# Optimization experiments

Hardware: AMD Instinct MI355X
Metric: run time of the kernel (lower is better)

Reference implementation:

```python
import jax, jax.numpy as jnp
import numpy as np
from jax import lax

IOU_THRESHOLD = 0.1
B, N = 4, 8192


def setup_inputs() -> dict:
    key = jax.random.key(0)
    # [B, 5, N]: rows 0..3 = cx, cy, w, h; row 4 = confidence score in (0, 1)
    outputs = jax.random.uniform(key, (B, 5, N), dtype=jnp.float32)
    return {"outputs": outputs}


def _nms_single(p):
    """Greedy NMS on one image. p: [5, N] -> [5, N] with kept boxes
    compacted to the front (original column order preserved) and the rest
    zero-padded. Matches the torch loop: repeatedly take the highest-scoring
    surviving box, drop all boxes with IoU >= threshold (box keeps itself),
    and drop boxes with score <= 0."""
    boxes, scores = p[:4], p[4]
    n = scores.shape[0]
    order = jnp.argsort(-scores)            # descending score order
    b = boxes[:, order]

    x1 = b[0] - b[2] * 0.5
    y1 = b[1] - b[3] * 0.5
    x2 = b[0] + b[2] * 0.5
    y2 = b[1] + b[3] * 0.5
    area = (x2 - x1) * (y2 - y1)

    iw = jnp.clip(jnp.minimum(x2[:, None], x2[None, :]) - jnp.maximum(x1[:, None], x1[None, :]), 0.0)
    ih = jnp.clip(jnp.minimum(y2[:, None], y2[None, :]) - jnp.maximum(y1[:, None], y1[None, :]), 0.0)
    inter = iw * ih
    union = area[:, None] + area[None, :] - inter
    iou = inter / (union + 1e-8)            # [N, N] in sorted order

    idx_range = jnp.arange(n)
    keep_init = scores[order] > 0           # non_zero_scores filter

    def body(i, keep):
        # if box i (in score order) survives, suppress j with IoU >= thr, j != i
        row_keep = (iou[i] < IOU_THRESHOLD) | (idx_range == i)
        return jnp.where(keep[i], keep & row_keep, keep)

    keep_sorted = lax.fori_loop(0, n, body, keep_init)

    # map keep mask back to original column order
    keep_orig = jnp.zeros((n,), bool).at[order].set(keep_sorted)
    # stable compaction: kept columns first, original relative order preserved
    perm = jnp.argsort(jnp.where(keep_orig, 0, 1), stable=True)
    gathered = p[:, perm]                    # [5, N]
    valid = idx_range < jnp.sum(keep_orig)
    return jnp.where(valid[None, :], gathered, 0.0)


def reference(outputs):
    # torch version pads to the max detections across the batch; here we keep
    # the fixed width N (extra columns are zero), same kept values/order.
    return jax.vmap(_nms_single)(outputs)


if __name__ == "__main__":
    inp = setup_inputs()
    out = jax.jit(reference)(**inp)
    print(out.shape, out.dtype)
```

## Files before the change

### kernel.cpp

```cpp
#include <hip/hip_runtime.h>

#pragma clang fp contract(off)

#define NBOX 8192
#define BLK  1024
#define EPT  8
#define NBUCK 2048
#define NB 256
#define IOU_THR 0.1f

typedef unsigned short u16;
typedef unsigned int u32;
typedef unsigned long long u64;

#define SMEM_TOT 160896

__global__ __launch_bounds__(BLK, 4) void nms_kernel(const float* __restrict__ in,
                                                     float* __restrict__ out) {
    __shared__ __align__(16) char smem[SMEM_TOT];
    const int img = blockIdx.x;
    const float* __restrict__ p = in + (size_t)img * 5 * NBOX;
    float* __restrict__ o = out + (size_t)img * 5 * NBOX;
    const int t = threadIdx.x;
    const int lane = t & 63;
    const int wid = t >> 6;

    float4* box   = (float4*)smem;
    u16* A        = (u16*)(smem + 131072);
    float4* bx    = (float4*)(smem + 147456);
    u64 (*mat)[4] = (u64(*)[4])(smem + 151552);
    float4* kx    = (float4*)(smem + 151552);
    u32* pfxA     = (u32*)(smem + 155648);
    u32* kom      = (u32*)(smem + 159744);
    int* wcnt     = (int*)(smem + 160768);
    u64* keptQ    = (u64*)(smem + 160832);
    int* S0sh     = (int*)(smem + 160864);
    u64* skey  = (u64*)smem;
    u32* hist  = (u32*)(smem + 65536);
    u32* bbase = (u32*)(smem + 73728);

    for (int i = t; i < NBUCK; i += BLK) hist[i] = 0;
    if (t < 256) kom[t] = 0;
    if (t == 0) *S0sh = 0;
    __syncthreads();

    u32 mybkt[EPT], myarr[EPT], mykeyhi[EPT];
#pragma unroll
    for (int e = 0; e < EPT; e++) {
        int j = t + e * BLK;
        float s = p[4 * NBOX + j];
        u32 u = __float_as_uint(s);
        u32 ordb = u ^ (u32)(((int)u >> 31) | (int)0x80000000);
        mykeyhi[e] = ~ordb;
        int vb = (int)(s * (float)NBUCK);
        vb = vb < 0 ? 0 : (vb > NBUCK - 1 ? NBUCK - 1 : vb);
        mybkt[e] = (u32)(NBUCK - 1 - vb);
        myarr[e] = atomicAdd(&hist[mybkt[e]], 1u);
        u64 bal = __ballot(s > 0.0f);
        if (lane == 0) atomicAdd(S0sh, (int)__popcll(bal));
    }
    __syncthreads();

    {
        u32 h0 = hist[2 * t], h1 = hist[2 * t + 1];
        int v = (int)(h0 + h1);
        int x = v;
        for (int d = 1; d < 64; d <<= 1) {
            int y = __shfl_up(x, d, 64);
            if (lane >= d) x += y;
        }
        if (lane == 63) wcnt[wid] = x;
        __syncthreads();
        int wb = 0;
        for (int i = 0; i < wid; i++) wb += wcnt[i];
        int excl = wb + x - v;
        bbase[2 * t] = (u32)excl;
        bbase[2 * t + 1] = (u32)excl + h0;
    }
    __syncthreads();

#pragma unroll
    for (int e = 0; e < EPT; e++) {
        u32 pos = bbase[mybkt[e]] + myarr[e];
        skey[pos] = ((u64)mykeyhi[e] << 32) | (u32)(t + e * BLK);
    }
    __syncthreads();

#pragma unroll
    for (int e = 0; e < EPT; e++) {
        u32 b = mybkt[e];
        u32 lo = bbase[b], hi2 = lo + hist[b];
        u64 me = ((u64)mykeyhi[e] << 32) | (u32)(t + e * BLK);
        u32 r = lo;
        for (u32 q = lo; q < hi2; q++) r += (skey[q] < me) ? 1u : 0u;
        A[r] = (u16)(t + e * BLK);
    }
    __syncthreads();
    int S = *S0sh;

#pragma unroll
    for (int e = 0; e < EPT; e++) {
        int j = t + e * BLK;
        float cx = p[j], cy = p[NBOX + j];
        float w_ = p[2 * NBOX + j], h_ = p[3 * NBOX + j];
        box[j] = make_float4(cx - w_ * 0.5f, cy - h_ * 0.5f,
                             cx + w_ * 0.5f, cy + h_ * 0.5f);
    }
    __syncthreads();

    if (t < NB) bx[t] = box[A[t]];
    __syncthreads();

    while (S > 0) {
        int nb = S < NB ? S : NB;

        {
            int i = t >> 2, ws = t & 3;
            if (i < nb) {
                float4 bi = bx[i];
                float ari = (bi.z - bi.x) * (bi.w - bi.y);
                u64 bits = 0;
                int c0 = ws * 64;
                int cmax = nb - c0; if (cmax > 64) cmax = 64;
                for (int cc = 0; cc < cmax; cc++) {
                    int c = c0 + cc;
                    float4 bc = bx[c];
                    float arc = (bc.z - bc.x) * (bc.w - bc.y);
                    float iw = fminf(bi.z, bc.z) - fmaxf(bi.x, bc.x);
                    float ih = fminf(bi.w, bc.w) - fmaxf(bi.y, bc.y);
                    if (c != i && iw > 0.0f && ih > 0.0f) {
                        float inter = iw * ih;
                        float uni = ari + arc - inter;
                        if (inter / (uni + 1e-8f) >= IOU_THR) bits |= (1ull << cc);
                    }
                }
                mat[i][ws] = bits;
            }
        }
        __syncthreads();

        if (wid == 0) {
            u64 r0[4], r1[4], r2[4], r3[4];
#pragma unroll
            for (int wq = 0; wq < 4; wq++) {
                r0[wq] = mat[lane][wq];
                r1[wq] = mat[64 + lane][wq];
                r2[wq] = mat[128 + lane][wq];
                r3[wq] = mat[192 + lane][wq];
            }
            u64 A0, A1, A2, A3;
            {
                int n0 = nb;       A0 = n0 <= 0 ? 0ull : (n0 >= 64 ? ~0ull : ((1ull << n0) - 1ull));
                int n1 = nb - 64;  A1 = n1 <= 0 ? 0ull : (n1 >= 64 ? ~0ull : ((1ull << n1) - 1ull));
                int n2 = nb - 128; A2 = n2 <= 0 ? 0ull : (n2 >= 64 ? ~0ull : ((1ull << n2) - 1ull));
                int n3 = nb - 192; A3 = n3 <= 0 ? 0ull : (n3 >= 64 ? ~0ull : ((1ull << n3) - 1ull));
            }
            u64 K0 = 0, K1 = 0, K2 = 0, K3 = 0;
            u64 lm = (1ull << lane) - 1ull;
            while (A0 | A1 | A2 | A3) {
                bool c0b = ((A0 >> lane) & 1) && !(r0[0] & A0 & lm);
                bool c1b = ((A1 >> lane) & 1) && !((r1[0] & A0) | (r1[1] & A1 & lm));
                bool c2b = ((A2 >> lane) & 1) && !((r2[0] & A0) | (r2[1] & A1) | (r2[2] & A2 & lm));
                bool c3b = ((A3 >> lane) & 1) && !((r3[0] & A0) | (r3[1] & A1) | (r3[2] & A2) | (r3[3] & A3 & lm));
                u64 C0 = __ballot(c0b), C1 = __ballot(c1b), C2 = __ballot(c2b), C3 = __ballot(c3b);
                K0 |= C0; K1 |= C1; K2 |= C2; K3 |= C3;
                A0 &= ~C0; A1 &= ~C1; A2 &= ~C2; A3 &= ~C3;
                bool s0b = ((A0 >> lane) & 1) && ((r0[0] & C0) | (r0[1] & C1) | (r0[2] & C2) | (r0[3] & C3));
                bool s1b = ((A1 >> lane) & 1) && ((r1[0] & C0) | (r1[1] & C1) | (r1[2] & C2) | (r1[3] & C3));
                bool s2b = ((A2 >> lane) & 1) && ((r2[0] & C0) | (r2[1] & C1) | (r2[2] & C2) | (r2[3] & C3));
                bool s3b = ((A3 >> lane) & 1) && ((r3[0] & C0) | (r3[1] & C1) | (r3[2] & C2) | (r3[3] & C3));
                A0 &= ~__ballot(s0b); A1 &= ~__ballot(s1b); A2 &= ~__ballot(s2b); A3 &= ~__ballot(s3b);
            }
            if (lane < 4) keptQ[lane] = lane == 0 ? K0 : lane == 1 ? K1 : lane == 2 ? K2 : K3;
        }
        __syncthreads();

        u64 kq0 = keptQ[0], kq1 = keptQ[1], kq2 = keptQ[2], kq3 = keptQ[3];
        int nk = (int)(__popcll(kq0) + __popcll(kq1) + __popcll(kq2) + __popcll(kq3));
        if (t < nb) {
            int wq = t >> 6;
            u64 kq = wq == 0 ? kq0 : wq == 1 ? kq1 : wq == 2 ? kq2 : kq3;
            if ((kq >> (t & 63)) & 1) {
                int j = (int)A[t];
                atomicOr(&kom[j >> 5], 1u << (j & 31));
                int pk = 0;
                if (wq > 0) pk += (int)__popcll(kq0);
                if (wq > 1) pk += (int)__popcll(kq1);
                if (wq > 2) pk += (int)__popcll(kq2);
                pk += (int)__popcll(kq & ((1ull << (t & 63)) - 1ull));
                kx[pk] = bx[t];
            }
        }
        int tailN = S - nb;
        int C = (tailN + BLK - 1) / BLK;
        int st = nb + t * C;
        int en = st + C; if (en > S) en = S;
        float4 eb[EPT]; float ea[EPT]; u16 ei[EPT];
        u32 am = 0;
#pragma unroll
        for (int e = 0; e < EPT; e++) {
            int pos = st + e;
            if (e < C && pos < en) {
                u16 j = A[pos];
                ei[e] = j;
                float4 b = box[j];
                eb[e] = b;
                ea[e] = (b.z - b.x) * (b.w - b.y);
                am |= (1u << e);
            }
        }
        __syncthreads();

        if (am) {
            for (int c = 0; c < nk; c++) {
                float4 cb = kx[c];
                float arc = (cb.z - cb.x) * (cb.w - cb.y);
#pragma unroll
                for (int e = 0; e < EPT; e++) {
                    if (am & (1u << e)) {
                        float iw = fminf(eb[e].z, cb.z) - fmaxf(eb[e].x, cb.x);
                        float ih = fminf(eb[e].w, cb.w) - fmaxf(eb[e].y, cb.y);
                        if (iw > 0.0f && ih > 0.0f) {
                            float inter = iw * ih;
                            float uni = ea[e] + arc - inter;
                            if (inter / (uni + 1e-8f) >= IOU_THR) am &= ~(1u << e);
                        }
                    }
                }
                if (!am) break;
            }
        }

        {
            int cnt = __popc(am);
            int x = cnt;
            for (int d = 1; d < 64; d <<= 1) {
                int y = __shfl_up(x, d, 64);
                if (lane >= d) x += y;
            }
            if (lane == 63) wcnt[wid] = x;
            __syncthreads();
            int wb = 0, tot = 0;
            for (int i = 0; i < BLK / 64; i++) {
                int v = wcnt[i];
                if (i < wid) wb += v;
                tot += v;
            }
            int off = wb + x - cnt;
#pragma unroll
            for (int e = 0; e < EPT; e++) {
                if (am & (1u << e)) {
                    A[off] = ei[e];
                    if (off < NB) bx[off] = eb[e];
                    off++;
                }
            }
            __syncthreads();
            S = tot;
        }
    }
    __syncthreads();

    {
        float4 z; z.x = z.y = z.z = z.w = 0.0f;
        float4* o4 = (float4*)o;
        for (int i = t; i < 5 * NBOX / 4; i += BLK) o4[i] = z;
    }
    {
        u32 w = (t < 256) ? kom[t] : 0u;
        int c = __popc(w);
        int x = c;
        for (int d = 1; d < 64; d <<= 1) {
            int y = __shfl_up(x, d, 64);
            if (lane >= d) x += y;
        }
        if (lane == 63) wcnt[wid] = x;
        __syncthreads();
        int wb = 0;
        for (int i = 0; i < wid; i++) wb += wcnt[i];
        if (t < 256) pfxA[t] = (u32)(wb + x - c);
    }
    __syncthreads();
    for (int j = t; j < NBOX; j += BLK) {
        u32 km = kom[j >> 5];
        if ((km >> (j & 31)) & 1u) {
            int pos = (int)(pfxA[j >> 5] + (u32)__popc(km & ((1u << (j & 31)) - 1u)));
            o[0 * NBOX + pos] = p[0 * NBOX + j];
            o[1 * NBOX + pos] = p[1 * NBOX + j];
            o[2 * NBOX + pos] = p[2 * NBOX + j];
            o[3 * NBOX + pos] = p[3 * NBOX + j];
            o[4 * NBOX + pos] = p[4 * NBOX + j];
        }
    }
}

extern "C" void kernel_launch(void* const* d_in, const int* in_sizes, int n_in,
                              void* d_out, int out_size, void* d_ws, size_t ws_size,
                              hipStream_t stream) {
    const float* in = (const float*)d_in[0];
    float* out = (float*)d_out;
    int B = in_sizes[0] / (5 * NBOX);
    hipLaunchKernelGGL(nms_kernel, dim3(B), dim3(BLK), 0, stream, in, out);
}
```

Before: 185.1 us.

## Sort kept boxes by area, rotate tile scan, precompute areas, zero output early

Kept boxes in each block are now rank-sorted by descending area before the tail suppression pass, so large boxes that suppress many candidates are tested first and the early exit fires sooner. Their areas are also stored in shared memory instead of being recomputed in the inner loop. The in-block IoU matrix loop now runs a fixed 64 iterations with a per-lane rotated column start, likely to spread LDS bank accesses, and is unrolled by 4. The output zeroing moves to the start of the kernel so it overlaps other work. The costs are an extra O(nk^2) rank pass plus a barrier per round, and slightly more shared memory.

New measurement: 197.4 us. 1.07x slower.

```diff
diff --git a/kernel.cpp b/kernel.cpp
--- a/kernel.cpp
+++ b/kernel.cpp
@@ -13,7 +13,7 @@
 typedef unsigned int u32;
 typedef unsigned long long u64;
 
-#define SMEM_TOT 160896
+#define SMEM_TOT 162944
 
 __global__ __launch_bounds__(BLK, 4) void nms_kernel(const float* __restrict__ in,
                                                      float* __restrict__ out) {
@@ -30,14 +30,24 @@
     float4* bx    = (float4*)(smem + 147456);
     u64 (*mat)[4] = (u64(*)[4])(smem + 151552);
     float4* kx    = (float4*)(smem + 151552);
-    u32* pfxA     = (u32*)(smem + 155648);
+    float4* kxS   = (float4*)(smem + 155648);
     u32* kom      = (u32*)(smem + 159744);
     int* wcnt     = (int*)(smem + 160768);
     u64* keptQ    = (u64*)(smem + 160832);
     int* S0sh     = (int*)(smem + 160864);
+    float* kaS    = (float*)(smem + 160896);
+    u32* pfxA     = (u32*)(smem + 160896);
+    float* kaF    = (float*)(smem + 161920);
     u64* skey  = (u64*)smem;
     u32* hist  = (u32*)(smem + 65536);
     u32* bbase = (u32*)(smem + 73728);
+
+    {
+        float4 z; z.x = z.y = z.z = z.w = 0.0f;
+        float4* o4 = (float4*)o;
+#pragma unroll
+        for (int e = 0; e < 10; e++) o4[t + e * BLK] = z;
+    }
 
     for (int i = t; i < NBUCK; i += BLK) hist[i] = 0;
     if (t < 256) kom[t] = 0;
@@ -121,17 +131,20 @@
                 float ari = (bi.z - bi.x) * (bi.w - bi.y);
                 u64 bits = 0;
                 int c0 = ws * 64;
-                int cmax = nb - c0; if (cmax > 64) cmax = 64;
-                for (int cc = 0; cc < cmax; cc++) {
-                    int c = c0 + cc;
-                    float4 bc = bx[c];
-                    float arc = (bc.z - bc.x) * (bc.w - bc.y);
-                    float iw = fminf(bi.z, bc.z) - fmaxf(bi.x, bc.x);
-                    float ih = fminf(bi.w, bc.w) - fmaxf(bi.y, bc.y);
-                    if (c != i && iw > 0.0f && ih > 0.0f) {
-                        float inter = iw * ih;
-                        float uni = ari + arc - inter;
-                        if (inter / (uni + 1e-8f) >= IOU_THR) bits |= (1ull << cc);
+#pragma unroll 4
+                for (int cc = 0; cc < 64; cc++) {
+                    int ccr = (cc + 2 * ws) & 63;
+                    int c = c0 + ccr;
+                    if (c < nb && c != i) {
+                        float4 bc = bx[c];
+                        float arc = (bc.z - bc.x) * (bc.w - bc.y);
+                        float iw = fminf(bi.z, bc.z) - fmaxf(bi.x, bc.x);
+                        float ih = fminf(bi.w, bc.w) - fmaxf(bi.y, bc.y);
+                        if (iw > 0.0f && ih > 0.0f) {
+                            float inter = iw * ih;
+                            float uni = ari + arc - inter;
+                            if (inter / (uni + 1e-8f) >= IOU_THR) bits |= (1ull << ccr);
+                        }
                     }
                 }
                 mat[i][ws] = bits;
@@ -188,7 +201,9 @@
                 if (wq > 1) pk += (int)__popcll(kq1);
                 if (wq > 2) pk += (int)__popcll(kq2);
                 pk += (int)__popcll(kq & ((1ull << (t & 63)) - 1ull));
-                kx[pk] = bx[t];
+                float4 b = bx[t];
+                kxS[pk] = b;
+                kaS[pk] = (b.z - b.x) * (b.w - b.y);
             }
         }
         int tailN = S - nb;
@@ -211,10 +226,23 @@
         }
         __syncthreads();
 
+        if (t < nk) {
+            float aq = kaS[t];
+            float4 bq = kxS[t];
+            int rk = 0;
+            for (int c = 0; c < nk; c++) {
+                float ac = kaS[c];
+                rk += (ac > aq) || (ac == aq && c < t) ? 1 : 0;
+            }
+            kx[rk] = bq;
+            kaF[rk] = aq;
+        }
+        __syncthreads();
+
         if (am) {
             for (int c = 0; c < nk; c++) {
                 float4 cb = kx[c];
-                float arc = (cb.z - cb.x) * (cb.w - cb.y);
+                float arc = kaF[c];
 #pragma unroll
                 for (int e = 0; e < EPT; e++) {
                     if (am & (1u << e)) {
@@ -262,11 +290,6 @@
     __syncthreads();
 
     {
-        float4 z; z.x = z.y = z.z = z.w = 0.0f;
-        float4* o4 = (float4*)o;
-        for (int i = t; i < 5 * NBOX / 4; i += BLK) o4[i] = z;
-    }
-    {
         u32 w = (t < 256) ? kom[t] : 0u;
         int c = __popc(w);
         int x = c;
```
